# Kernel optimization log

Hardware: AMD Instinct MI355X
Metric: run time of the kernel (lower is better)

## Reference

```python
import jax, jax.numpy as jnp
import numpy as np

FG_THRESH = 0.5
BG_THRESH_HI = 0.5
BG_THRESH_LO = 0.1


def _bbox_overlaps(boxes, query):
    x1 = jnp.maximum(boxes[:, None, 0], query[None, :, 0])
    y1 = jnp.maximum(boxes[:, None, 1], query[None, :, 1])
    x2 = jnp.minimum(boxes[:, None, 2], query[None, :, 2])
    y2 = jnp.minimum(boxes[:, None, 3], query[None, :, 3])
    iw = jnp.clip(x2 - x1 + 1.0, 0.0)
    ih = jnp.clip(y2 - y1 + 1.0, 0.0)
    inter = iw * ih  # [N,C]
    area_b = (boxes[:, 2] - boxes[:, 0] + 1.0) * (boxes[:, 3] - boxes[:, 1] + 1.0)
    area_q = (query[:, 2] - query[:, 0] + 1.0) * (query[:, 3] - query[:, 1] + 1.0)
    return inter / (area_b[:, None] + area_q[None, :] - inter)


def _refine_supervision(prob, ss_boxes, pos_mask, IS_weight):
    # vectorized, fully on-device version of get_refine_supervision
    C = pos_mask.shape[0]
    p = jax.lax.stop_gradient(prob * IS_weight)  # original detaches via .data.cpu().numpy()
    if p.shape[1] == C + 1:
        p = p[:, 1:]  # drop background column
    max_idx = jnp.argmax(p, axis=0)                     # [C] top-scoring roi per class
    boxes_c = jax.lax.stop_gradient(ss_boxes)[max_idx, 1:5]  # [C,4] pseudo-GT boxes
    ov = _bbox_overlaps(jax.lax.stop_gradient(ss_boxes)[:, 1:5], boxes_c)  # [N,C]
    ov = jnp.where(pos_mask[None, :], ov, -1.0)         # only image-level positive classes
    gt = jnp.argmax(ov, axis=1)                         # [N] assignment
    mo = jnp.max(ov, axis=1)                            # [N] max overlap
    fg = mo > FG_THRESH
    bg = (mo >= BG_THRESH_LO) & (mo < BG_THRESH_HI)
    keep = fg | bg                                      # keep_inds as a mask
    col = jnp.where(fg, gt + 1, 0)                      # one-hot column per kept roi
    return keep, col


def _refine_loss(refine_prob, keep, col, IS_weight):
    n = jnp.sum(keep).astype(refine_prob.dtype)
    lp = jnp.take_along_axis(jnp.log(refine_prob), col[:, None], axis=1)[:, 0]  # [N]
    return -jnp.sum(jnp.where(keep, IS_weight[:, 0] * lp, 0.0)) / n


def reference(fc7_roi, fc7_context, fc7_frame, W_cls, b_cls, W_det, b_det,
              W_r1, b_r1, W_r2, b_r2, ss_boxes, IS_weight, image_level_label):
    C = W_cls.shape[1]
    cls_score = fc7_roi @ W_cls + b_cls                       # [N,C]
    det_score = (fc7_frame @ W_det + b_det) - (fc7_context @ W_det + b_det)  # frame - context
    refine_prob_1 = jax.nn.softmax(fc7_roi @ W_r1 + b_r1, axis=1)  # [N,C+1]
    refine_prob_2 = jax.nn.softmax(fc7_roi @ W_r2 + b_r2, axis=1)
    cls_prob = jax.nn.softmax(cls_score, axis=1)
    det_prob = jax.nn.softmax(det_score, axis=0)              # softmax over rois
    det_cls_prob_product = cls_prob * det_prob                # [N,C]
    det_cls_score = jnp.sum(cls_score * det_prob, axis=0)     # [C]

    pos_mask = image_level_label[0] == 1                      # [C]
    keep1, col1 = _refine_supervision(det_cls_prob_product, ss_boxes, pos_mask, IS_weight)
    refine_loss_1 = _refine_loss(refine_prob_1, keep1, col1, IS_weight)
    keep2, col2 = _refine_supervision(refine_prob_1, ss_boxes, pos_mask, IS_weight)
    refine_loss_2 = _refine_loss(refine_prob_2, keep2, col2, IS_weight)

    lab = image_level_label[0].astype(det_cls_score.dtype)    # +/-1 labels
    cls_det_loss = jnp.sum(jnp.maximum(0.0, 1.0 - lab * det_cls_score)) / C
    total_loss = cls_det_loss + 0.1 * refine_loss_1 + 0.1 * refine_loss_2
    return total_loss


def setup_inputs() -> dict:
    key = jax.random.key(0)
    ks = jax.random.split(key, 16)
    N, F, C = 4096, 4096, 20
    s = 0.01  # weight scale to keep softmax/hinge well-conditioned
    fc7_roi = jax.random.normal(ks[0], (N, F), jnp.float32)
    fc7_context = jax.random.normal(ks[1], (N, F), jnp.float32)
    fc7_frame = jax.random.normal(ks[2], (N, F), jnp.float32)
    W_cls = jax.random.normal(ks[3], (F, C), jnp.float32) * s
    W_det = jax.random.normal(ks[4], (F, C), jnp.float32) * s
    W_r1 = jax.random.normal(ks[5], (F, C + 1), jnp.float32) * s
    W_r2 = jax.random.normal(ks[6], (F, C + 1), jnp.float32) * s
    b_cls = jnp.zeros((C,), jnp.float32)
    b_det = jnp.zeros((C,), jnp.float32)
    b_r1 = jnp.zeros((C + 1,), jnp.float32)
    b_r2 = jnp.zeros((C + 1,), jnp.float32)
    x1 = jax.random.uniform(ks[7], (N,), jnp.float32, 0.0, 500.0)
    y1 = jax.random.uniform(ks[8], (N,), jnp.float32, 0.0, 500.0)
    w = jax.random.uniform(ks[9], (N,), jnp.float32, 10.0, 120.0)
    h = jax.random.uniform(ks[10], (N,), jnp.float32, 10.0, 120.0)
    ss_boxes = jnp.stack([jnp.zeros((N,), jnp.float32), x1, y1, x1 + w, y1 + h], axis=1)
    IS_weight = jax.random.uniform(ks[11], (N, 1), jnp.float32, 0.5, 1.0)
    lbl = jnp.where(jax.random.bernoulli(ks[12], 0.4, (1, C)), 1, -1).astype(jnp.int32)
    lbl = lbl.at[0, 0].set(1)  # guarantee at least one positive class
    return {"fc7_roi": fc7_roi, "fc7_context": fc7_context, "fc7_frame": fc7_frame,
            "W_cls": W_cls, "b_cls": b_cls, "W_det": W_det, "b_det": b_det,
            "W_r1": W_r1, "b_r1": b_r1, "W_r2": W_r2, "b_r2": b_r2,
            "ss_boxes": ss_boxes, "IS_weight": IS_weight, "image_level_label": lbl}
```

## Files before the change

### kernel.cpp

```cpp
#include <hip/hip_runtime.h>

typedef __attribute__((ext_vector_type(4))) float f32x4;
typedef __attribute__((ext_vector_type(8))) short short8;
typedef __attribute__((ext_vector_type(4))) unsigned int u32x4;

#define N_ROWS 4096
#define KDIM   4096
#define NC     96
#define GSPLIT 16

__device__ inline short f2bf(float f) {
  unsigned u = __builtin_bit_cast(unsigned, f);
  u += 0x7FFFu + ((u >> 16) & 1u);
  return (short)(u >> 16);
}

__device__ inline unsigned cvtpk(float lo, float hi) {
  unsigned r;
  asm("v_cvt_pk_bf16_f32 %0, %1, %2" : "=v"(r) : "v"(lo), "v"(hi));
  return r;
}

__global__ void k_pack(const float* __restrict__ Wcls, const float* __restrict__ Wr1,
                       const float* __restrict__ Wr2, const float* __restrict__ Wdet,
                       ushort* __restrict__ Wp) {
  int t = blockIdx.x * 256 + threadIdx.x;
  int K = t / 3072;
  int rem = t - K * 3072;
  int ct = rem >> 9;
  int rem2 = rem & 511;
  int l = rem2 >> 3;
  int j = rem2 & 7;
  int k = K * 32 + (l >> 4) * 8 + j;
  int col = ct * 16 + (l & 15);
  float v = 0.f;
  if (col < 20)                 v = Wcls[k * 20 + col];
  else if (col < 41)            v = Wr1[k * 21 + (col - 20)];
  else if (col < 62)            v = Wr2[k * 21 + (col - 41)];
  else if (col >= 64 && col < 84) v = Wdet[k * 20 + (col - 64)];
  Wp[t] = (ushort)f2bf(v);
}

#define GLo(dst, base, OFF) \
  asm volatile("global_load_dwordx4 %0, %1, off offset:%c2" : "=v"(dst) : "v"(base), "i"(OFF) : "memory")
#define WAITV(N) asm volatile("s_waitcnt vmcnt(" #N ")" ::: "memory")
#define SB() __builtin_amdgcn_sched_barrier(0)

#define ISSUEA(KS, BF) do {                              \
    GLo(raw[BF][0], pr, (KS)*128);                       \
    GLo(raw[BF][1], pr, (KS)*128 + 16);                  \
    GLo(raw[BF][2], pf, (KS)*128);                       \
    GLo(raw[BF][3], pf, (KS)*128 + 16);                  \
    GLo(raw[BF][4], pc, (KS)*128);                       \
    GLo(raw[BF][5], pc, (KS)*128 + 16);                  \
  } while (0)

__global__ __launch_bounds__(256, 3) void k_gemm(const float* __restrict__ roi,
    const float* __restrict__ frame, const float* __restrict__ ctx,
    const ushort* __restrict__ Wp, float* __restrict__ Spart) {
  const int t    = threadIdx.x;
  const int lane = t & 63;
  const int wid  = t >> 6;
  const int rb   = blockIdx.x >> 4;
  const int g    = blockIdx.x & 15;

  __shared__ alignas(16) ushort smemB[8 * 6 * 64 * 8];

  {
    const ushort* src = Wp + (size_t)g * 24576;
    for (int r = 0; r < 12; ++r) {
      const int e = r * 256 + t;
      *(short8*)(&smemB[e * 8]) = *(const short8*)(src + e * 8);
    }
  }
  __syncthreads();

  const int row = rb * 64 + wid * 16 + (lane & 15);
  const size_t aoff = (size_t)row * KDIM + g * 256 + (lane >> 4) * 8;
  const float* pr = roi   + aoff;
  const float* pf = frame + aoff;
  const float* pc = ctx   + aoff;

  f32x4 raw[3][6];
  f32x4 acc[6];
#pragma unroll
  for (int i = 0; i < 6; ++i) acc[i] = (f32x4){0.f, 0.f, 0.f, 0.f};

  ISSUEA(0, 0);
  ISSUEA(1, 1);

#pragma unroll
  for (int ks = 0; ks < 8; ++ks) {
    if (ks < 6) ISSUEA(ks + 2, (ks + 2) % 3);
    if (ks < 6)      { WAITV(12); }
    else if (ks == 6){ WAITV(6); }
    else             { WAITV(0); }
    SB();
    const f32x4* c = raw[ks % 3];
    u32x4 uR, uD;
    uR.x = cvtpk(c[0][0], c[0][1]); uR.y = cvtpk(c[0][2], c[0][3]);
    uR.z = cvtpk(c[1][0], c[1][1]); uR.w = cvtpk(c[1][2], c[1][3]);
    uD.x = cvtpk(c[2][0] - c[4][0], c[2][1] - c[4][1]);
    uD.y = cvtpk(c[2][2] - c[4][2], c[2][3] - c[4][3]);
    uD.z = cvtpk(c[3][0] - c[5][0], c[3][1] - c[5][1]);
    uD.w = cvtpk(c[3][2] - c[5][2], c[3][3] - c[5][3]);
    const short8 aR = __builtin_bit_cast(short8, uR);
    const short8 aD = __builtin_bit_cast(short8, uD);
#pragma unroll
    for (int ct = 0; ct < 6; ++ct) {
      const short8 b = *(const short8*)(&smemB[((ks * 6 + ct) * 64 + lane) * 8]);
      acc[ct] = __builtin_amdgcn_mfma_f32_16x16x32_bf16(ct < 4 ? aR : aD, b, acc[ct], 0, 0, 0);
    }
  }

  float* out = Spart + (size_t)g * (N_ROWS * NC) + (size_t)(rb * 64 + wid * 16) * NC;
  const int rbase = (lane >> 4) * 4;
  const int col = lane & 15;
#pragma unroll
  for (int ct = 0; ct < 6; ++ct)
#pragma unroll
    for (int r = 0; r < 4; ++r)
      out[(size_t)(rbase + r) * NC + ct * 16 + col] = acc[ct][r];
}

__global__ void k_rr(const float* __restrict__ Spart, const float* __restrict__ bcls,
    const float* __restrict__ br1, const float* __restrict__ br2,
    float* __restrict__ S, float* __restrict__ clsp, float* __restrict__ rp1,
    float* __restrict__ lse1, float* __restrict__ lse2) {
  const int b = blockIdx.x;
  const int t = threadIdx.x;
  const int base = b * 3072;
#pragma unroll
  for (int j = 0; j < 12; ++j) {
    const int e = base + j * 256 + t;
    float s = 0.f;
#pragma unroll
    for (int gg = 0; gg < GSPLIT; ++gg) s += Spart[(size_t)gg * (N_ROWS * NC) + e];
    S[e] = s;
  }
  __syncthreads();
  if (t < 32) {
    const int i = b * 32 + t;
    const float* sr = S + (size_t)i * NC;
    float s[21];
    float m = -3.4e38f;
    for (int c = 0; c < 20; ++c) { s[c] = sr[c] + bcls[c]; m = fmaxf(m, s[c]); }
    float sum = 0.f;
    for (int c = 0; c < 20; ++c) { float e = expf(s[c] - m); s[c] = e; sum += e; }
    float inv = 1.f / sum;
    for (int c = 0; c < 20; ++c) clsp[(size_t)i * 20 + c] = s[c] * inv;
    m = -3.4e38f;
    for (int c = 0; c < 21; ++c) { s[c] = sr[20 + c] + br1[c]; m = fmaxf(m, s[c]); }
    sum = 0.f;
    for (int c = 0; c < 21; ++c) { float e = expf(s[c] - m); s[c] = e; sum += e; }
    lse1[i] = m + logf(sum);
    inv = 1.f / sum;
    for (int c = 0; c < 21; ++c) rp1[(size_t)i * 21 + c] = s[c] * inv;
    m = -3.4e38f;
    for (int c = 0; c < 21; ++c) { s[c] = sr[41 + c] + br2[c]; m = fmaxf(m, s[c]); }
    sum = 0.f;
    for (int c = 0; c < 21; ++c) sum += expf(s[c] - m);
    lse2[i] = m + logf(sum);
  }
}

__global__ __launch_bounds__(256) void k_col(const float* __restrict__ S,
    const float* __restrict__ clsp, const float* __restrict__ rp1,
    const float* __restrict__ isw, const float* __restrict__ ssb,
    const float* __restrict__ bcls,
    float* __restrict__ dcs, float* __restrict__ b1out, float* __restrict__ b2out) {
  const int c = blockIdx.x;
  const int t = threadIdx.x;
  __shared__ float rv[256];
  __shared__ int ri[256];
  float m = -3.4e38f;
  for (int i = t; i < N_ROWS; i += 256) m = fmaxf(m, S[(size_t)i * NC + 64 + c]);
  rv[t] = m; __syncthreads();
  for (int o = 128; o; o >>= 1) { if (t < o) rv[t] = fmaxf(rv[t], rv[t + o]); __syncthreads(); }
  const float M = rv[0]; __syncthreads();
  float se = 0.f, scd = 0.f, v1b = -3.4e38f, v2b = -3.4e38f;
  int i1 = 0, i2 = 0;
  for (int i = t; i < N_ROWS; i += 256) {
    float w = isw[i];
    float e = expf(S[(size_t)i * NC + 64 + c] - M);
    se += e;
    scd += (S[(size_t)i * NC + c] + bcls[c]) * e;
    float v1 = clsp[(size_t)i * 20 + c] * e * w;
    if (v1 > v1b) { v1b = v1; i1 = i; }
    float v2 = rp1[(size_t)i * 21 + c + 1] * w;
    if (v2 > v2b) { v2b = v2; i2 = i; }
  }
  rv[t] = se; __syncthreads();
  for (int o = 128; o; o >>= 1) { if (t < o) rv[t] += rv[t + o]; __syncthreads(); }
  const float SE = rv[0]; __syncthreads();
  rv[t] = scd; __syncthreads();
  for (int o = 128; o; o >>= 1) { if (t < o) rv[t] += rv[t + o]; __syncthreads(); }
  const float SCD = rv[0]; __syncthreads();
  rv[t] = v1b; ri[t] = i1; __syncthreads();
  for (int o = 128; o; o >>= 1) {
    if (t < o) { if (rv[t + o] > rv[t] || (rv[t + o] == rv[t] && ri[t + o] < ri[t])) { rv[t] = rv[t + o]; ri[t] = ri[t + o]; } }
    __syncthreads();
  }
  const int I1 = ri[0]; __syncthreads();
  rv[t] = v2b; ri[t] = i2; __syncthreads();
  for (int o = 128; o; o >>= 1) {
    if (t < o) { if (rv[t + o] > rv[t] || (rv[t + o] == rv[t] && ri[t + o] < ri[t])) { rv[t] = rv[t + o]; ri[t] = ri[t + o]; } }
    __syncthreads();
  }
  const int I2 = ri[0];
  if (t == 0) {
    dcs[c] = SCD / SE;
    for (int q = 0; q < 4; ++q) {
      b1out[c * 4 + q] = ssb[(size_t)I1 * 5 + 1 + q];
      b2out[c * 4 + q] = ssb[(size_t)I2 * 5 + 1 + q];
    }
  }
}

__global__ __launch_bounds__(256) void k_sup(const float* __restrict__ S,
    const float* __restrict__ ssb, const float* __restrict__ isw,
    const int* __restrict__ label,
    const float* __restrict__ b1in, const float* __restrict__ b2in,
    const float* __restrict__ lse1, const float* __restrict__ lse2,
    const float* __restrict__ br1, const float* __restrict__ br2,
    float* __restrict__ scal) {
  __shared__ float q1[20][4], q2[20][4], a1[20], a2[20];
  __shared__ int pos[20];
  const int t = threadIdx.x;
  if (t < 20) {
    for (int q = 0; q < 4; ++q) { q1[t][q] = b1in[t * 4 + q]; q2[t][q] = b2in[t * 4 + q]; }
    a1[t] = (q1[t][2] - q1[t][0] + 1.f) * (q1[t][3] - q1[t][1] + 1.f);
    a2[t] = (q2[t][2] - q2[t][0] + 1.f) * (q2[t][3] - q2[t][1] + 1.f);
    pos[t] = (label[t] == 1);
  }
  __syncthreads();
  const int i = blockIdx.x * 256 + t;
  const float bx1 = ssb[(size_t)i * 5 + 1], by1 = ssb[(size_t)i * 5 + 2];
  const float bx2 = ssb[(size_t)i * 5 + 3], by2 = ssb[(size_t)i * 5 + 4];
  const float ab = (bx2 - bx1 + 1.f) * (by2 - by1 + 1.f);
  const float w = isw[i];
  float p1 = 0.f, n1 = 0.f, p2 = 0.f, n2 = 0.f;
  {
    float mo = -2.f; int gt = 0;
    for (int c = 0; c < 20; ++c) {
      float v = -1.f;
      if (pos[c]) {
        float xx1 = fmaxf(bx1, q1[c][0]), yy1 = fmaxf(by1, q1[c][1]);
        float xx2 = fminf(bx2, q1[c][2]), yy2 = fminf(by2, q1[c][3]);
        float iw = fmaxf(xx2 - xx1 + 1.f, 0.f), ih = fmaxf(yy2 - yy1 + 1.f, 0.f);
        float inter = iw * ih;
        v = inter / (ab + a1[c] - inter);
      }
      if (v > mo) { mo = v; gt = c; }
    }
    bool fg = mo > 0.5f;
    bool bg = (mo >= 0.1f) && (mo < 0.5f);
    if (fg || bg) {
      int col = fg ? gt + 1 : 0;
      float lp = S[(size_t)i * NC + 20 + col] + br1[col] - lse1[i];
      p1 = w * lp; n1 = 1.f;
    }
  }
  {
    float mo = -2.f; int gt = 0;
    for (int c = 0; c < 20; ++c) {
      float v = -1.f;
      if (pos[c]) {
        float xx1 = fmaxf(bx1, q2[c][0]), yy1 = fmaxf(by1, q2[c][1]);
        float xx2 = fminf(bx2, q2[c][2]), yy2 = fminf(by2, q2[c][3]);
        float iw = fmaxf(xx2 - xx1 + 1.f, 0.f), ih = fmaxf(yy2 - yy1 + 1.f, 0.f);
        float inter = iw * ih;
        v = inter / (ab + a2[c] - inter);
      }
      if (v > mo) { mo = v; gt = c; }
    }
    bool fg = mo > 0.5f;
    bool bg = (mo >= 0.1f) && (mo < 0.5f);
    if (fg || bg) {
      int col = fg ? gt + 1 : 0;
      float lp = S[(size_t)i * NC + 41 + col] + br2[col] - lse2[i];
      p2 = w * lp; n2 = 1.f;
    }
  }
  __shared__ float rs[256];
  float sums[4] = {p1, n1, p2, n2};
  float tot[4];
  for (int q = 0; q < 4; ++q) {
    rs[t] = sums[q]; __syncthreads();
    for (int o = 128; o; o >>= 1) { if (t < o) rs[t] += rs[t + o]; __syncthreads(); }
    tot[q] = rs[0]; __syncthreads();
  }
  if (t == 0) {
    atomicAdd(&scal[0], tot[0]); atomicAdd(&scal[1], tot[1]);
    atomicAdd(&scal[2], tot[2]); atomicAdd(&scal[3], tot[3]);
  }
}

__global__ void k_final(const float* __restrict__ dcs, const int* __restrict__ label,
                        const float* __restrict__ scal, float* __restrict__ out) {
  if (threadIdx.x == 0 && blockIdx.x == 0) {
    float cd = 0.f;
    for (int c = 0; c < 20; ++c) {
      float lab = (float)label[c];
      cd += fmaxf(1.f - lab * dcs[c], 0.f);
    }
    cd *= (1.f / 20.f);
    float rl1 = -scal[0] / scal[1];
    float rl2 = -scal[2] / scal[3];
    out[0] = cd + 0.1f * (rl1 + rl2);
  }
}

constexpr size_t OFF_S     = 0;
constexpr size_t OFF_SCAL  = OFF_S + (size_t)N_ROWS * NC * 4;
constexpr size_t OFF_DCS   = OFF_SCAL + 16;
constexpr size_t OFF_B1    = OFF_DCS + 80;
constexpr size_t OFF_B2    = OFF_B1 + 320;
constexpr size_t OFF_LSE1  = OFF_B2 + 320;
constexpr size_t OFF_LSE2  = OFF_LSE1 + 16384;
constexpr size_t OFF_CLSP  = OFF_LSE2 + 16384;
constexpr size_t OFF_RP1   = OFF_CLSP + 327680;
constexpr size_t OFF_WP    = OFF_RP1 + 344064;
constexpr size_t OFF_SPART = OFF_WP + 786432;

extern "C" void kernel_launch(void* const* d_in, const int* in_sizes, int n_in,
                              void* d_out, int out_size, void* d_ws, size_t ws_size,
                              hipStream_t stream) {
  const float* roi   = (const float*)d_in[0];
  const float* ctx   = (const float*)d_in[1];
  const float* frame = (const float*)d_in[2];
  const float* Wcls  = (const float*)d_in[3];
  const float* bcls  = (const float*)d_in[4];
  const float* Wdet  = (const float*)d_in[5];
  const float* Wr1   = (const float*)d_in[7];
  const float* br1   = (const float*)d_in[8];
  const float* Wr2   = (const float*)d_in[9];
  const float* br2   = (const float*)d_in[10];
  const float* ssb   = (const float*)d_in[11];
  const float* isw   = (const float*)d_in[12];
  const int*   label = (const int*)d_in[13];

  char* ws = (char*)d_ws;
  float*  S     = (float*)(ws + OFF_S);
  float*  scal  = (float*)(ws + OFF_SCAL);
  float*  dcs   = (float*)(ws + OFF_DCS);
  float*  b1    = (float*)(ws + OFF_B1);
  float*  b2    = (float*)(ws + OFF_B2);
  float*  lse1  = (float*)(ws + OFF_LSE1);
  float*  lse2  = (float*)(ws + OFF_LSE2);
  float*  clsp  = (float*)(ws + OFF_CLSP);
  float*  rp1   = (float*)(ws + OFF_RP1);
  ushort* Wp    = (ushort*)(ws + OFF_WP);
  float*  Spart = (float*)(ws + OFF_SPART);

  hipMemsetAsync(scal, 0, 16, stream);
  k_pack<<<1536, 256, 0, stream>>>(Wcls, Wr1, Wr2, Wdet, Wp);
  k_gemm<<<1024, 256, 0, stream>>>(roi, frame, ctx, Wp, Spart);
  k_rr<<<128, 256, 0, stream>>>(Spart, bcls, br1, br2, S, clsp, rp1, lse1, lse2);
  k_col<<<20, 256, 0, stream>>>(S, clsp, rp1, isw, ssb, bcls, dcs, b1, b2);
  k_sup<<<16, 256, 0, stream>>>(S, ssb, isw, label, b1, b2, lse1, lse2, br1, br2, scal);
  k_final<<<1, 64, 0, stream>>>(dcs, label, scal, (float*)d_out);
}
```

Before: 90.72 us.

## Stage A tiles via global_load_lds with swizzle, shrink K-split to 4

Result: faster. 84.62 us (-6.7%).

```diff
diff --git a/kernel.cpp b/kernel.cpp
--- a/kernel.cpp
+++ b/kernel.cpp
@@ -7,7 +7,7 @@
 #define N_ROWS 4096
 #define KDIM   4096
 #define NC     96
-#define GSPLIT 16
+#define GSPLIT 4
 
 __device__ inline short f2bf(float f) {
   unsigned u = __builtin_bit_cast(unsigned, f);
@@ -19,6 +19,12 @@
   unsigned r;
   asm("v_cvt_pk_bf16_f32 %0, %1, %2" : "=v"(r) : "v"(lo), "v"(hi));
   return r;
+}
+
+typedef const __attribute__((address_space(1))) void gas_t;
+typedef __attribute__((address_space(3))) void las_t;
+__device__ __forceinline__ void gll16(const float* g, void* l) {
+  __builtin_amdgcn_global_load_lds((gas_t*)g, (las_t*)l, 16, 0, 0);
 }
 
 __global__ void k_pack(const float* __restrict__ Wcls, const float* __restrict__ Wr1,
@@ -41,86 +47,106 @@
   Wp[t] = (ushort)f2bf(v);
 }
 
-#define GLo(dst, base, OFF) \
-  asm volatile("global_load_dwordx4 %0, %1, off offset:%c2" : "=v"(dst) : "v"(base), "i"(OFF) : "memory")
 #define WAITV(N) asm volatile("s_waitcnt vmcnt(" #N ")" ::: "memory")
 #define SB() __builtin_amdgcn_sched_barrier(0)
-
-#define ISSUEA(KS, BF) do {                              \
-    GLo(raw[BF][0], pr, (KS)*128);                       \
-    GLo(raw[BF][1], pr, (KS)*128 + 16);                  \
-    GLo(raw[BF][2], pf, (KS)*128);                       \
-    GLo(raw[BF][3], pf, (KS)*128 + 16);                  \
-    GLo(raw[BF][4], pc, (KS)*128);                       \
-    GLo(raw[BF][5], pc, (KS)*128 + 16);                  \
+#define ABUF(P) ((P) == 0 ? bufA0 : (P) == 1 ? bufA1 : bufA2)
+
+#define STAGE_A(C) do {                                                       \
+    char* _b = ABUF((C) % 3);                                                 \
+    _Pragma("unroll") for (int m = 0; m < 3; ++m) {                           \
+      const float* _s = (m == 0 ? pR : m == 1 ? pF : pX) + (size_t)(C) * 64;  \
+      _Pragma("unroll") for (int i = 0; i < 4; ++i)                           \
+        gll16(_s + (size_t)i * 4 * KDIM, _b + m * 4096 + i * 1024);           \
+    }                                                                         \
   } while (0)
 
-__global__ __launch_bounds__(256, 3) void k_gemm(const float* __restrict__ roi,
+#define STAGE_B(C) do {                                                       \
+    _Pragma("unroll") for (int q = 0; q < 12; ++q)                            \
+      Bv[(C) & 1][q] = *(const short8*)(pb + (size_t)(C) * 6144 +             \
+                                        (q / 6) * 3072 + (q % 6) * 512);      \
+  } while (0)
+
+#define LDA(P, M, KS, H)                                                      \
+  (*(const f32x4*)(ABUF(P) + (M) * 4096 + base2 +                             \
+                   ((((KS) * 8 + kg * 2 + (H)) ^ r3) << 4)))
+
+#define COMPUTE(C) do {                                                       \
+    _Pragma("unroll") for (int ks2 = 0; ks2 < 2; ++ks2) {                     \
+      f32x4 r0 = LDA((C) % 3, 0, ks2, 0), r1 = LDA((C) % 3, 0, ks2, 1);       \
+      f32x4 f0 = LDA((C) % 3, 1, ks2, 0), f1 = LDA((C) % 3, 1, ks2, 1);       \
+      f32x4 x0 = LDA((C) % 3, 2, ks2, 0), x1 = LDA((C) % 3, 2, ks2, 1);       \
+      u32x4 uR, uD;                                                           \
+      uR.x = cvtpk(r0[0], r0[1]); uR.y = cvtpk(r0[2], r0[3]);                 \
+      uR.z = cvtpk(r1[0], r1[1]); uR.w = cvtpk(r1[2], r1[3]);                 \
+      uD.x = cvtpk(f0[0] - x0[0], f0[1] - x0[1]);                             \
+      uD.y = cvtpk(f0[2] - x0[2], f0[3] - x0[3]);                             \
+      uD.z = cvtpk(f1[0] - x1[0], f1[1] - x1[1]);                             \
+      uD.w = cvtpk(f1[2] - x1[2], f1[3] - x1[3]);                             \
+      const short8 aR = __builtin_bit_cast(short8, uR);                       \
+      const short8 aD = __builtin_bit_cast(short8, uD);                       \
+      _Pragma("unroll") for (int ct = 0; ct < 6; ++ct)                        \
+        acc[ct] = __builtin_amdgcn_mfma_f32_16x16x32_bf16(                    \
+            ct < 4 ? aR : aD, Bv[(C) & 1][ks2 * 6 + ct], acc[ct], 0, 0, 0);   \
+    }                                                                         \
+  } while (0)
+
+#define CHUNK(C, NW) do {                                                     \
+    if ((C) + 1 <= 15) { STAGE_B((C) + 1); SB(); }                            \
+    if ((C) + 2 <= 15) { STAGE_A((C) + 2); SB(); }                            \
+    WAITV(NW); SB();                                                          \
+    COMPUTE(C);                                                               \
+  } while (0)
+
+__global__ __launch_bounds__(64, 1) void k_gemm(const float* __restrict__ roi,
     const float* __restrict__ frame, const float* __restrict__ ctx,
     const ushort* __restrict__ Wp, float* __restrict__ Spart) {
-  const int t    = threadIdx.x;
-  const int lane = t & 63;
-  const int wid  = t >> 6;
-  const int rb   = blockIdx.x >> 4;
-  const int g    = blockIdx.x & 15;
-
-  __shared__ alignas(16) ushort smemB[8 * 6 * 64 * 8];
-
-  {
-    const ushort* src = Wp + (size_t)g * 24576;
-    for (int r = 0; r < 12; ++r) {
-      const int e = r * 256 + t;
-      *(short8*)(&smemB[e * 8]) = *(const short8*)(src + e * 8);
-    }
-  }
-  __syncthreads();
-
-  const int row = rb * 64 + wid * 16 + (lane & 15);
-  const size_t aoff = (size_t)row * KDIM + g * 256 + (lane >> 4) * 8;
-  const float* pr = roi   + aoff;
-  const float* pf = frame + aoff;
-  const float* pc = ctx   + aoff;
-
-  f32x4 raw[3][6];
+  __shared__ alignas(16) char bufA0[12288];
+  __shared__ alignas(16) char bufA1[12288];
+  __shared__ alignas(16) char bufA2[12288];
+  const int l  = threadIdx.x;
+  const int rt = blockIdx.x >> 2;
+  const int g  = blockIdx.x & 3;
+
+  const int rlhi = l >> 4;
+  const int sw = (l & 15) ^ (rlhi & 3);
+  const size_t srow = (size_t)(rt * 16 + rlhi) * KDIM + (size_t)g * 1024 + sw * 4;
+  const float* pR = roi + srow;
+  const float* pF = frame + srow;
+  const float* pX = ctx + srow;
+  const ushort* pb = Wp + (size_t)g * 32 * 3072 + l * 8;
+
+  const int rl = l & 15, kg = l >> 4, r3 = rl & 3;
+  const unsigned base2 = (unsigned)((rl >> 2) * 1024 + r3 * 256);
+
+  short8 Bv[2][12];
   f32x4 acc[6];
 #pragma unroll
   for (int i = 0; i < 6; ++i) acc[i] = (f32x4){0.f, 0.f, 0.f, 0.f};
 
-  ISSUEA(0, 0);
-  ISSUEA(1, 1);
-
-#pragma unroll
-  for (int ks = 0; ks < 8; ++ks) {
-    if (ks < 6) ISSUEA(ks + 2, (ks + 2) % 3);
-    if (ks < 6)      { WAITV(12); }
-    else if (ks == 6){ WAITV(6); }
-    else             { WAITV(0); }
-    SB();
-    const f32x4* c = raw[ks % 3];
-    u32x4 uR, uD;
-    uR.x = cvtpk(c[0][0], c[0][1]); uR.y = cvtpk(c[0][2], c[0][3]);
-    uR.z = cvtpk(c[1][0], c[1][1]); uR.w = cvtpk(c[1][2], c[1][3]);
-    uD.x = cvtpk(c[2][0] - c[4][0], c[2][1] - c[4][1]);
-    uD.y = cvtpk(c[2][2] - c[4][2], c[2][3] - c[4][3]);
-    uD.z = cvtpk(c[3][0] - c[5][0], c[3][1] - c[5][1]);
-    uD.w = cvtpk(c[3][2] - c[5][2], c[3][3] - c[5][3]);
-    const short8 aR = __builtin_bit_cast(short8, uR);
-    const short8 aD = __builtin_bit_cast(short8, uD);
-#pragma unroll
-    for (int ct = 0; ct < 6; ++ct) {
-      const short8 b = *(const short8*)(&smemB[((ks * 6 + ct) * 64 + lane) * 8]);
-      acc[ct] = __builtin_amdgcn_mfma_f32_16x16x32_bf16(ct < 4 ? aR : aD, b, acc[ct], 0, 0, 0);
-    }
-  }
-
-  float* out = Spart + (size_t)g * (N_ROWS * NC) + (size_t)(rb * 64 + wid * 16) * NC;
-  const int rbase = (lane >> 4) * 4;
-  const int col = lane & 15;
+  STAGE_A(0); SB();
+  STAGE_B(0); SB();
+  STAGE_A(1); SB();
+
+  CHUNK(0, 36);  CHUNK(1, 36);  CHUNK(2, 36);  CHUNK(3, 36);
+  CHUNK(4, 36);  CHUNK(5, 36);  CHUNK(6, 36);  CHUNK(7, 36);
+  CHUNK(8, 36);  CHUNK(9, 36);  CHUNK(10, 36); CHUNK(11, 36);
+  CHUNK(12, 36); CHUNK(13, 36); CHUNK(14, 24); CHUNK(15, 0);
+
+  float* red = (float*)bufA0;
+  const int rbase = (l >> 4) * 4;
+  const int col = l & 15;
 #pragma unroll
   for (int ct = 0; ct < 6; ++ct)
 #pragma unroll
     for (int r = 0; r < 4; ++r)
-      out[(size_t)(rbase + r) * NC + ct * 16 + col] = acc[ct][r];
+      red[(rbase + r) * NC + ct * 16 + col] = acc[ct][r];
+  asm volatile("s_waitcnt lgkmcnt(0)" ::: "memory"); SB();
+  float* outp = Spart + (size_t)g * (N_ROWS * NC) + (size_t)rt * (16 * NC);
+#pragma unroll
+  for (int q = 0; q < 6; ++q) {
+    f32x4 v = *(const f32x4*)(red + l * 24 + q * 4);
+    *(f32x4*)(outp + l * 24 + q * 4) = v;
+  }
 }
 
 __global__ void k_rr(const float* __restrict__ Spart, const float* __restrict__ bcls,
@@ -355,7 +381,7 @@
 
   hipMemsetAsync(scal, 0, 16, stream);
   k_pack<<<1536, 256, 0, stream>>>(Wcls, Wr1, Wr2, Wdet, Wp);
-  k_gemm<<<1024, 256, 0, stream>>>(roi, frame, ctx, Wp, Spart);
+  k_gemm<<<1024, 64, 0, stream>>>(roi, frame, ctx, Wp, Spart);
   k_rr<<<128, 256, 0, stream>>>(Spart, bcls, br1, br2, S, clsp, rp1, lse1, lse2);
   k_col<<<20, 256, 0, stream>>>(S, clsp, rp1, isw, ssb, bcls, dcs, b1, b2);
   k_sup<<<16, 256, 0, stream>>>(S, ssb, isw, label, b1, b2, lse1, lse2, br1, br2, scal);
```

## Stage GEMM A tiles through LDS with direct global-to-LDS loads, fewer K splits

Applied to the files above, without the earlier changes.

Result: slower. 112.7 us (+24.3%).

```diff
diff --git a/kernel.cpp b/kernel.cpp
--- a/kernel.cpp
+++ b/kernel.cpp
@@ -7,7 +7,9 @@
 #define N_ROWS 4096
 #define KDIM   4096
 #define NC     96
-#define GSPLIT 16
+#define GSPLIT 2
+#define NCH    16
+#define CK     128
 
 __device__ inline short f2bf(float f) {
   unsigned u = __builtin_bit_cast(unsigned, f);
@@ -19,6 +21,21 @@
   unsigned r;
   asm("v_cvt_pk_bf16_f32 %0, %1, %2" : "=v"(r) : "v"(lo), "v"(hi));
   return r;
+}
+
+typedef const __attribute__((address_space(1))) void gas_t;
+typedef __attribute__((address_space(3))) void las_t;
+__device__ __forceinline__ void gll16(const float* g, void* l) {
+  __builtin_amdgcn_global_load_lds((gas_t*)g, (las_t*)l, 16, 0, 0);
+}
+
+__global__ __launch_bounds__(256) void k_probe(const float* __restrict__ r, float* __restrict__ out) {
+  const size_t i = (size_t)blockIdx.x * 256 + threadIdx.x;
+  f32x4 s = (f32x4){0.f, 0.f, 0.f, 0.f};
+#pragma unroll
+  for (int j = 0; j < 8; ++j)
+    s += *(const f32x4*)(r + (i + (size_t)j * 524288) * 4);
+  out[i] = s[0] + s[1] + s[2] + s[3];
 }
 
 __global__ void k_pack(const float* __restrict__ Wcls, const float* __restrict__ Wr1,
@@ -41,86 +58,112 @@
   Wp[t] = (ushort)f2bf(v);
 }
 
-#define GLo(dst, base, OFF) \
-  asm volatile("global_load_dwordx4 %0, %1, off offset:%c2" : "=v"(dst) : "v"(base), "i"(OFF) : "memory")
 #define WAITV(N) asm volatile("s_waitcnt vmcnt(" #N ")" ::: "memory")
 #define SB() __builtin_amdgcn_sched_barrier(0)
-
-#define ISSUEA(KS, BF) do {                              \
-    GLo(raw[BF][0], pr, (KS)*128);                       \
-    GLo(raw[BF][1], pr, (KS)*128 + 16);                  \
-    GLo(raw[BF][2], pf, (KS)*128);                       \
-    GLo(raw[BF][3], pf, (KS)*128 + 16);                  \
-    GLo(raw[BF][4], pc, (KS)*128);                       \
-    GLo(raw[BF][5], pc, (KS)*128 + 16);                  \
+#define BUFSEL(C) (((C) & 1) ? buf1 : buf0)
+#define BVSEL(C)  (((C) & 1) ? Bv1 : Bv0)
+
+#define ISSUE_A(C) do {                                                        \
+    char* _d = BUFSEL(C);                                                      \
+    _Pragma("unroll") for (int m = 0; m < 3; ++m)                              \
+      _Pragma("unroll") for (int p = 0; p < 2; ++p)                            \
+        gll16(pA[m][p] + (C) * CK, _d + m * 8192 + (w * 4 + 2 * p) * 512);     \
   } while (0)
 
-__global__ __launch_bounds__(256, 3) void k_gemm(const float* __restrict__ roi,
+#define ISSUE_B(C) do {                                                        \
+    short8* _bv = BVSEL(C);                                                    \
+    const ushort* _p = pb + (size_t)(C) * 12288;                               \
+    _Pragma("unroll") for (int ct = 0; ct < 6; ++ct)                           \
+      _bv[ct] = *(const short8*)(_p + ct * 512);                               \
+  } while (0)
+
+#define COMPUTE(C) do {                                                        \
+    const char* _b = BUFSEL(C); const short8* _bv = BVSEL(C);                  \
+    f32x4 r0 = *(const f32x4*)(_b + rl * 512 + (((gb + 0) ^ rx) << 4));        \
+    f32x4 r1 = *(const f32x4*)(_b + rl * 512 + (((gb + 1) ^ rx) << 4));        \
+    f32x4 f0 = *(const f32x4*)(_b + 8192 + rl * 512 + (((gb + 0) ^ rx) << 4)); \
+    f32x4 f1 = *(const f32x4*)(_b + 8192 + rl * 512 + (((gb + 1) ^ rx) << 4)); \
+    f32x4 x0 = *(const f32x4*)(_b + 16384 + rl * 512 + (((gb + 0) ^ rx) << 4));\
+    f32x4 x1 = *(const f32x4*)(_b + 16384 + rl * 512 + (((gb + 1) ^ rx) << 4));\
+    u32x4 uR, uD;                                                              \
+    uR.x = cvtpk(r0[0], r0[1]); uR.y = cvtpk(r0[2], r0[3]);                    \
+    uR.z = cvtpk(r1[0], r1[1]); uR.w = cvtpk(r1[2], r1[3]);                    \
+    uD.x = cvtpk(f0[0] - x0[0], f0[1] - x0[1]);                                \
+    uD.y = cvtpk(f0[2] - x0[2], f0[3] - x0[3]);                                \
+    uD.z = cvtpk(f1[0] - x1[0], f1[1] - x1[1]);                                \
+    uD.w = cvtpk(f1[2] - x1[2], f1[3] - x1[3]);                                \
+    const short8 aR = __builtin_bit_cast(short8, uR);                          \
+    const short8 aD = __builtin_bit_cast(short8, uD);                          \
+    _Pragma("unroll") for (int ct = 0; ct < 6; ++ct)                           \
+      acc[ct] = __builtin_amdgcn_mfma_f32_16x16x32_bf16(                       \
+          ct < 4 ? aR : aD, _bv[ct], acc[ct], 0, 0, 0);                        \
+  } while (0)
+
+#define CHUNKI(C, NW) do {                                                     \
+    WAITV(NW); SB();                                                           \
+    __builtin_amdgcn_s_barrier(); SB();                                        \
+    COMPUTE(C); SB();                                                          \
+    __builtin_amdgcn_s_barrier(); SB();                                        \
+    if ((C) + 2 < NCH) { ISSUE_A((C) + 2); ISSUE_B((C) + 2); SB(); }           \
+  } while (0)
+
+__global__ __launch_bounds__(256) void k_gemm(const float* __restrict__ roi,
     const float* __restrict__ frame, const float* __restrict__ ctx,
     const ushort* __restrict__ Wp, float* __restrict__ Spart) {
+  __shared__ alignas(16) char buf0[24576];
+  __shared__ alignas(16) char buf1[24576];
   const int t    = threadIdx.x;
   const int lane = t & 63;
-  const int wid  = t >> 6;
-  const int rb   = blockIdx.x >> 4;
-  const int g    = blockIdx.x & 15;
-
-  __shared__ alignas(16) ushort smemB[8 * 6 * 64 * 8];
-
-  {
-    const ushort* src = Wp + (size_t)g * 24576;
-    for (int r = 0; r < 12; ++r) {
-      const int e = r * 256 + t;
-      *(short8*)(&smemB[e * 8]) = *(const short8*)(src + e * 8);
-    }
-  }
+  const int w    = t >> 6;
+  const int rt   = blockIdx.x & 255;
+  const int g    = blockIdx.x >> 8;
+
+  const int lrow = lane >> 5, lgr = lane & 31;
+  const float* pA[3][2];
+#pragma unroll
+  for (int m = 0; m < 3; ++m)
+#pragma unroll
+    for (int p = 0; p < 2; ++p) {
+      const int rloc = w * 4 + 2 * p + lrow;
+      const int gran = lgr ^ (rloc & 7);
+      const float* mat = (m == 0 ? roi : m == 1 ? frame : ctx);
+      pA[m][p] = mat + (size_t)(rt * 16 + rloc) * KDIM + (size_t)g * (NCH * CK) + gran * 4;
+    }
+  const ushort* pb = Wp + (size_t)(g * 64 + w) * 3072 + lane * 8;
+
+  const int rl = lane & 15, kg = lane >> 4;
+  const unsigned rx = (unsigned)(rl & 7);
+  const unsigned gb = (unsigned)(w * 8 + kg * 2);
+
+  short8 Bv0[6], Bv1[6];
+  f32x4 acc[6];
+#pragma unroll
+  for (int i = 0; i < 6; ++i) acc[i] = (f32x4){0.f, 0.f, 0.f, 0.f};
+
+  ISSUE_A(0); ISSUE_B(0); SB();
+  ISSUE_A(1); ISSUE_B(1); SB();
+
+  CHUNKI(0, 12);  CHUNKI(1, 12);  CHUNKI(2, 12);  CHUNKI(3, 12);
+  CHUNKI(4, 12);  CHUNKI(5, 12);  CHUNKI(6, 12);  CHUNKI(7, 12);
+  CHUNKI(8, 12);  CHUNKI(9, 12);  CHUNKI(10, 12); CHUNKI(11, 12);
+  CHUNKI(12, 12); CHUNKI(13, 12); CHUNKI(14, 12); CHUNKI(15, 0);
+
   __syncthreads();
-
-  const int row = rb * 64 + wid * 16 + (lane & 15);
-  const size_t aoff = (size_t)row * KDIM + g * 256 + (lane >> 4) * 8;
-  const float* pr = roi   + aoff;
-  const float* pf = frame + aoff;
-  const float* pc = ctx   + aoff;
-
-  f32x4 raw[3][6];
-  f32x4 acc[6];
-#pragma unroll
-  for (int i = 0; i < 6; ++i) acc[i] = (f32x4){0.f, 0.f, 0.f, 0.f};
-
-  ISSUEA(0, 0);
-  ISSUEA(1, 1);
-
-#pragma unroll
-  for (int ks = 0; ks < 8; ++ks) {
-    if (ks < 6) ISSUEA(ks + 2, (ks + 2) % 3);
-    if (ks < 6)      { WAITV(12); }
-    else if (ks == 6){ WAITV(6); }
-    else             { WAITV(0); }
-    SB();
-    const f32x4* c = raw[ks % 3];
-    u32x4 uR, uD;
-    uR.x = cvtpk(c[0][0], c[0][1]); uR.y = cvtpk(c[0][2], c[0][3]);
-    uR.z = cvtpk(c[1][0], c[1][1]); uR.w = cvtpk(c[1][2], c[1][3]);
-    uD.x = cvtpk(c[2][0] - c[4][0], c[2][1] - c[4][1]);
-    uD.y = cvtpk(c[2][2] - c[4][2], c[2][3] - c[4][3]);
-    uD.z = cvtpk(c[3][0] - c[5][0], c[3][1] - c[5][1]);
-    uD.w = cvtpk(c[3][2] - c[5][2], c[3][3] - c[5][3]);
-    const short8 aR = __builtin_bit_cast(short8, uR);
-    const short8 aD = __builtin_bit_cast(short8, uD);
-#pragma unroll
-    for (int ct = 0; ct < 6; ++ct) {
-      const short8 b = *(const short8*)(&smemB[((ks * 6 + ct) * 64 + lane) * 8]);
-      acc[ct] = __builtin_amdgcn_mfma_f32_16x16x32_bf16(ct < 4 ? aR : aD, b, acc[ct], 0, 0, 0);
-    }
-  }
-
-  float* out = Spart + (size_t)g * (N_ROWS * NC) + (size_t)(rb * 64 + wid * 16) * NC;
+  float* red = (float*)buf0;
   const int rbase = (lane >> 4) * 4;
   const int col = lane & 15;
 #pragma unroll
   for (int ct = 0; ct < 6; ++ct)
 #pragma unroll
     for (int r = 0; r < 4; ++r)
-      out[(size_t)(rbase + r) * NC + ct * 16 + col] = acc[ct][r];
+      red[(w * 16 + rbase + r) * NC + ct * 16 + col] = acc[ct][r];
+  __syncthreads();
+  float* outp = Spart + (size_t)g * (N_ROWS * NC) + (size_t)rt * (16 * NC);
+#pragma unroll
+  for (int q = 0; q < 6; ++q) {
+    const int e = t * 6 + q;
+    outp[e] = red[e] + red[1536 + e] + red[3072 + e] + red[4608 + e];
+  }
 }
 
 __global__ void k_rr(const float* __restrict__ Spart, const float* __restrict__ bcls,
@@ -322,6 +365,7 @@
 constexpr size_t OFF_RP1   = OFF_CLSP + 327680;
 constexpr size_t OFF_WP    = OFF_RP1 + 344064;
 constexpr size_t OFF_SPART = OFF_WP + 786432;
+constexpr size_t OFF_PROBE = OFF_SPART + (size_t)GSPLIT * N_ROWS * NC * 4;
 
 extern "C" void kernel_launch(void* const* d_in, const int* in_sizes, int n_in,
                               void* d_out, int out_size, void* d_ws, size_t ws_size,
@@ -352,10 +396,12 @@
   float*  rp1   = (float*)(ws + OFF_RP1);
   ushort* Wp    = (ushort*)(ws + OFF_WP);
   float*  Spart = (float*)(ws + OFF_SPART);
+  float*  probe = (float*)(ws + OFF_PROBE);
 
   hipMemsetAsync(scal, 0, 16, stream);
+  k_probe<<<2048, 256, 0, stream>>>(roi, probe);
   k_pack<<<1536, 256, 0, stream>>>(Wcls, Wr1, Wr2, Wdet, Wp);
-  k_gemm<<<1024, 256, 0, stream>>>(roi, frame, ctx, Wp, Spart);
+  k_gemm<<<512, 256, 0, stream>>>(roi, frame, ctx, Wp, Spart);
   k_rr<<<128, 256, 0, stream>>>(Spart, bcls, br1, br2, S, clsp, rp1, lse1, lse2);
   k_col<<<20, 256, 0, stream>>>(S, clsp, rp1, isw, ssb, bcls, dcs, b1, b2);
   k_sup<<<16, 256, 0, stream>>>(S, ssb, isw, label, b1, b2, lse1, lse2, br1, br2, scal);
```
